# Kernel optimization log

Hardware: AMD Instinct MI355X
Metric: run time of the kernel (lower is better)

Reference implementation:

```python
import jax, jax.numpy as jnp
import numpy as np

B, S, E, H = 2, 2048, 1024, 16
DH = E // H


def setup_inputs() -> dict:
    key = jax.random.key(0)
    ks = jax.random.split(key, 12)
    std = 1.0 / np.sqrt(E)
    inp = {
        "query": jax.random.normal(ks[0], (B, S, E), jnp.float32),
        "key": jax.random.normal(ks[1], (B, S, E), jnp.float32),
        "value": jax.random.normal(ks[2], (B, S, E), jnp.float32),
        "mask": jax.random.randint(ks[3], (B, 1, 1, S), 0, 2, jnp.int32),
        "Wq": jax.random.normal(ks[4], (E, E), jnp.float32) * std,
        "bq": jnp.zeros((E,), jnp.float32),
        "Wk": jax.random.normal(ks[5], (E, E), jnp.float32) * std,
        "bk": jnp.zeros((E,), jnp.float32),
        "Wv": jax.random.normal(ks[6], (E, E), jnp.float32) * std,
        "bv": jnp.zeros((E,), jnp.float32),
        "Wo": jax.random.normal(ks[7], (E, E), jnp.float32) * std,
        "bo": jnp.zeros((E,), jnp.float32),
    }
    return inp


def reference(query, key, value, mask, Wq, bq, Wk, bk, Wv, bv, Wo, bo):
    b = query.shape[0]
    # QKV projections, then split heads: [B,S,E] -> [B,H,S,Dh]
    def split_heads(x):
        return x.reshape(b, -1, H, DH).transpose(0, 2, 1, 3)
    q = split_heads(query @ Wq + bq)
    k = split_heads(key @ Wk + bk)
    v = split_heads(value @ Wv + bv)
    # explicit bmm -> mask -> softmax -> bmm (non-SDPA), scores [B,H,Sq,Sk]
    scores = jnp.einsum("bhqd,bhkd->bhqk", q, k) / np.sqrt(DH).astype(np.float32)
    scores = jnp.where(mask == 0, jnp.float32(-1e9), scores)
    attn = jax.nn.softmax(scores, axis=-1)  # dropout is identity in eval mode
    out = jnp.einsum("bhqk,bhkd->bhqd", attn, v)
    out = out.transpose(0, 2, 1, 3).reshape(b, -1, E)  # merge heads
    return out @ Wo + bo
```

## Files before the change

kernel.cpp:

```cpp
#include <hip/hip_runtime.h>
#include <hip/hip_bf16.h>
#include <stdint.h>

#define B_ 2
#define S_ 2048
#define E_ 1024
#define H_ 16
#define DH_ 64
#define MELEMS (4096 * 1024)
#define WE (1024 * 1024)

typedef unsigned short u16;
typedef __bf16 bf16x8 __attribute__((ext_vector_type(8)));
typedef u16 u16x8 __attribute__((ext_vector_type(8)));
typedef u16 u16x4 __attribute__((ext_vector_type(4)));
typedef float f32x4 __attribute__((ext_vector_type(4)));
typedef float f32x16 __attribute__((ext_vector_type(16)));
typedef uint32_t u32x4 __attribute__((ext_vector_type(4)));
typedef uint32_t u32x2v __attribute__((ext_vector_type(2)));

__device__ __forceinline__ float bf2f(u16 u) {
    union { uint32_t i; float f; } v; v.i = ((uint32_t)u) << 16; return v.f;
}
__device__ __forceinline__ u16 f2bf(float f) {
    union { float f; uint32_t i; } v; v.f = f;
    uint32_t r = (v.i + 0x7FFFu + ((v.i >> 16) & 1u)) >> 16;
    return (u16)r;
}
__device__ __forceinline__ uint32_t cvtpk(float a, float b) {
    uint32_t r;
    asm("v_cvt_pk_bf16_f32 %0, %1, %2" : "=v"(r) : "v"(a), "v"(b));
    return r;
}
__device__ __forceinline__ bf16x8 ldfrag(const u16* p) {
    u16x8 t = *(const u16x8*)p;
    return __builtin_bit_cast(bf16x8, t);
}
__device__ __forceinline__ void gld16(const void* g, void* l) {
    __builtin_amdgcn_global_load_lds(
        (const __attribute__((address_space(1))) void*)g,
        (__attribute__((address_space(3))) void*)l, 16, 0, 0);
}

__global__ __launch_bounds__(256)
void cvt_all(const float* __restrict__ q, const float* __restrict__ k,
             const float* __restrict__ v,
             const float* __restrict__ W0, const float* __restrict__ W1,
             const float* __restrict__ W2, const float* __restrict__ W3,
             u16* __restrict__ Qi, u16* __restrict__ Ki, u16* __restrict__ Vi,
             u16* __restrict__ T0, u16* __restrict__ T1,
             u16* __restrict__ T2, u16* __restrict__ T3)
{
    __shared__ float tile[64][65];
    const int bid = blockIdx.x;
    const int tid = threadIdx.x;

    if (bid < 6144) {
        const int z = bid >> 11;
        const int cx = bid & 2047;
        const float* src = (z == 0) ? q : (z == 1) ? k : v;
        u16* dst = (z == 0) ? Qi : (z == 1) ? Ki : Vi;
        const size_t i8 = ((size_t)cx * 256 + tid) * 8;
        float4 f0 = *(const float4*)&src[i8];
        float4 f1 = *(const float4*)&src[i8 + 4];
        u16x8 t;
        t[0] = f2bf(f0.x); t[1] = f2bf(f0.y); t[2] = f2bf(f0.z); t[3] = f2bf(f0.w);
        t[4] = f2bf(f1.x); t[5] = f2bf(f1.y); t[6] = f2bf(f1.z); t[7] = f2bf(f1.w);
        *(u16x8*)&dst[i8] = t;
    } else {
        const int rr = bid - 6144;
        const int z = rr >> 8;
        const int tt = rr & 255;
        const float* W = (z == 0) ? W0 : (z == 1) ? W1 : (z == 2) ? W2 : W3;
        u16* T = (z == 0) ? T0 : (z == 1) ? T1 : (z == 2) ? T2 : T3;
        const int n0 = (tt & 15) * 64, k0 = (tt >> 4) * 64;
        const int r = tid >> 2, c0 = (tid & 3) * 16;

        #pragma unroll
        for (int i = 0; i < 4; ++i) {
            float4 w = *(const float4*)&W[(size_t)(k0 + r) * 1024 + n0 + c0 + i * 4];
            tile[r][c0 + i * 4 + 0] = w.x; tile[r][c0 + i * 4 + 1] = w.y;
            tile[r][c0 + i * 4 + 2] = w.z; tile[r][c0 + i * 4 + 3] = w.w;
        }
        __syncthreads();
        u16x8 a, b;
        #pragma unroll
        for (int j = 0; j < 8; ++j) a[j] = f2bf(tile[c0 + j][r]);
        #pragma unroll
        for (int j = 0; j < 8; ++j) b[j] = f2bf(tile[c0 + 8 + j][r]);
        *(u16x8*)&T[(size_t)(n0 + r) * 1024 + k0 + c0] = a;
        *(u16x8*)&T[(size_t)(n0 + r) * 1024 + k0 + c0 + 8] = b;
    }
}

template<int BN>
__global__ __launch_bounds__(256)
void gemm_bt(const u16* __restrict__ A0, const u16* __restrict__ A1,
             const u16* __restrict__ A2,
             const u16* __restrict__ Bt0, const u16* __restrict__ Bt1,
             const u16* __restrict__ Bt2,
             const float* __restrict__ b0, const float* __restrict__ b1,
             const float* __restrict__ b2,
             void* __restrict__ C0, void* __restrict__ C1, void* __restrict__ C2,
             const int* __restrict__ mask,
             int c_f32, int vt_z, float scale0, int K)
{
    const int z = blockIdx.z;
    const u16* A  = (z == 0) ? A0 : (z == 1) ? A1 : A2;
    const u16* Bt = (z == 0) ? Bt0 : (z == 1) ? Bt1 : Bt2;
    const float* bias = (z == 0) ? b0 : (z == 1) ? b1 : b2;
    void* C = (z == 0) ? C0 : (z == 1) ? C1 : C2;
    const float scale = (z == 0) ? scale0 : 1.0f;

    __shared__ alignas(16) u16 As[128 * 32];
    __shared__ alignas(16) u16 Bs[BN * 32];

    const int tid  = threadIdx.x;
    const int lane = tid & 63;
    const int wv   = tid >> 6;
    const int l15  = lane & 15;
    const int quad = lane >> 4;

    const int nwg = gridDim.x * gridDim.y;
    int wg = blockIdx.y * gridDim.x + blockIdx.x;
    wg = (wg & 7) * (nwg >> 3) + (wg >> 3);
    const int bx = wg % gridDim.x;
    const int by = wg / gridDim.x;

    const int m0 = by * 128;
    const int n0 = bx * BN;
    const int wr = (wv >> 1) * 64;
    const int wc = (wv & 1) * (BN / 2);

    const int srow = wv * 16 + (lane >> 2);
    const int skk  = (lane & 3) * 8;

    constexpr int NJ = BN / 32;
    f32x4 acc[4][NJ] = {};

    for (int k0 = 0; k0 < K; k0 += 32) {
        __syncthreads();
        #pragma unroll
        for (int h = 0; h < 2; ++h) {
            const int r = h * 64 + srow;
            gld16(&A[(size_t)(m0 + r) * K + k0 + skk], &As[r * 32 + skk]);
        }
        #pragma unroll
        for (int h = 0; h < BN / 64; ++h) {
            const int r = h * 64 + srow;
            gld16(&Bt[(size_t)(n0 + r) * K + k0 + skk], &Bs[r * 32 + skk]);
        }
        __syncthreads();

        bf16x8 a[4], b[NJ];
        #pragma unroll
        for (int i = 0; i < 4; ++i)
            a[i] = ldfrag(&As[(wr + i * 16 + l15) * 32 + quad * 8]);
        #pragma unroll
        for (int j = 0; j < NJ; ++j)
            b[j] = ldfrag(&Bs[(wc + j * 16 + l15) * 32 + quad * 8]);
        #pragma unroll
        for (int i = 0; i < 4; ++i)
            #pragma unroll
            for (int j = 0; j < NJ; ++j)
                acc[i][j] = __builtin_amdgcn_mfma_f32_16x16x32_bf16(
                    a[i], b[j], acc[i][j], 0, 0, 0);
    }

    #pragma unroll
    for (int j = 0; j < NJ; ++j) {
        const int col = n0 + wc + j * 16 + l15;
        const float bcol = bias[col];
        #pragma unroll
        for (int i = 0; i < 4; ++i) {
            const int row0 = m0 + wr + i * 16 + quad * 4;
            if (z == vt_z) {
                const int bb = row0 >> 11, s0 = row0 & 2047;
                const int4 mv = *(const int4*)&mask[bb * S_ + s0];
                u16x4 t;
                t[0] = mv.x ? f2bf((acc[i][j][0] + bcol) * scale) : (u16)0;
                t[1] = mv.y ? f2bf((acc[i][j][1] + bcol) * scale) : (u16)0;
                t[2] = mv.z ? f2bf((acc[i][j][2] + bcol) * scale) : (u16)0;
                t[3] = mv.w ? f2bf((acc[i][j][3] + bcol) * scale) : (u16)0;
                *(u16x4*)&((u16*)C)[((size_t)bb * E_ + col) * S_ + s0] = t;
            } else {
                #pragma unroll
                for (int r = 0; r < 4; ++r) {
                    const int row = row0 + r;
                    const float v = (acc[i][j][r] + bcol) * scale;
                    if (c_f32) ((float*)C)[(size_t)row * 1024 + col] = v;
                    else       ((u16*)C)[(size_t)row * 1024 + col]  = f2bf(v);
                }
            }
        }
    }
}

__global__ __launch_bounds__(512, 4)
void attn_v15(const u16* __restrict__ Q, const u16* __restrict__ K,
              const u16* __restrict__ Vt_g, const int* __restrict__ mask,
              u16* __restrict__ ctx)
{
    __shared__ alignas(16) u16 smem[2][8192];
    __shared__ alignas(16) u16 Mbf[S_];
    __shared__ float scrl[256];

    const int tid  = threadIdx.x;
    const int lane = tid & 63;
    const int wv   = tid >> 6;
    const int l31  = lane & 31;
    const int half = lane >> 5;
    const int sw7  = lane & 7;
    const int qw   = wv & 3;
    const int kh   = wv >> 2;
    const int kbase = kh * 32;

    const int nwg = gridDim.x * gridDim.y;
    int wg = blockIdx.y * gridDim.x + blockIdx.x;
    wg = (wg & 7) * (nwg >> 3) + (wg >> 3);
    const int qt = wg % gridDim.x;
    const int bh = wg / gridDim.x;
    const int b  = bh >> 4, h = bh & 15;

    const size_t qk_off = (size_t)b * S_ * E_ + (size_t)h * DH_;
    const size_t vt_off = ((size_t)b * E_ + (size_t)h * DH_) * S_;
    const int* mrow = &mask[b * S_];

    {
        const int i = tid * 4;
        const int4 m = *(const int4*)&mrow[i];
        u16x4 t;
        t[0] = m.x ? (u16)0x3F80 : (u16)0;
        t[1] = m.y ? (u16)0x3F80 : (u16)0;
        t[2] = m.z ? (u16)0x3F80 : (u16)0;
        t[3] = m.w ? (u16)0x3F80 : (u16)0;
        *(u16x4*)&Mbf[i] = t;
    }

    const int q0 = qt * 128 + qw * 32;
    bf16x8 qf[4];
    #pragma unroll
    for (int s = 0; s < 4; ++s)
        qf[s] = ldfrag(&Q[qk_off + (size_t)(q0 + l31) * E_ + s * 16 + half * 8]);

    f32x16 O[2] = {};
    f32x16 lacc = {};

    auto stage = [&](int kc, int buf) {
        const int rr = tid >> 3;
        const int ks = tid & 7;
        const int gb = ks ^ (rr & 7);
        gld16(&K[qk_off + (size_t)(kc + rr) * E_ + gb * 8],
              &smem[buf][rr * 64 + ks * 8]);
        gld16(&Vt_g[vt_off + (size_t)rr * S_ + kc + gb * 8],
              &smem[buf][4096 + rr * 64 + ks * 8]);
    };

    stage(0, 0);
    int cur = 0;

    for (int kc = 0; kc < S_; kc += 64) {
        __syncthreads();
        if (kc + 64 < S_) stage(kc + 64, cur ^ 1);
        const u16* Kb = &smem[cur][0];
        const u16* Vb = &smem[cur][4096];

        __builtin_amdgcn_s_setprio(1);
        f32x16 St = {};
        #pragma unroll
        for (int s = 0; s < 4; ++s) {
            bf16x8 kf = ldfrag(&Kb[(kbase + l31) * 64 + ((s * 2 + half) ^ sw7) * 8]);
            St = __builtin_amdgcn_mfma_f32_32x32x16_bf16(kf, qf[s], St, 0, 0, 0);
        }
        __builtin_amdgcn_s_setprio(0);
        float ex[16];
        #pragma unroll
        for (int i = 0; i < 16; ++i) ex[i] = __builtin_exp2f(St[i]);

        uint32_t wd[8];
        #pragma unroll
        for (int i = 0; i < 8; ++i) wd[i] = cvtpk(ex[2 * i], ex[2 * i + 1]);

        u32x2v r02 = __builtin_amdgcn_permlane32_swap(wd[0], wd[2], false, false);
        u32x2v r13 = __builtin_amdgcn_permlane32_swap(wd[1], wd[3], false, false);
        u32x2v r46 = __builtin_amdgcn_permlane32_swap(wd[4], wd[6], false, false);
        u32x2v r57 = __builtin_amdgcn_permlane32_swap(wd[5], wd[7], false, false);
        u32x4 f0, f1;
        f0[0] = r02[0]; f0[1] = r13[0]; f0[2] = r02[1]; f0[3] = r13[1];
        f1[0] = r46[0]; f1[1] = r57[0]; f1[2] = r46[1]; f1[3] = r57[1];
        const bf16x8 pa0 = __builtin_bit_cast(bf16x8, f0);
        const bf16x8 pa1 = __builtin_bit_cast(bf16x8, f1);

        __builtin_amdgcn_s_setprio(1);
        {
            bf16x8 mb0 = ldfrag(&Mbf[kc + kbase + half * 8]);
            bf16x8 mb1 = ldfrag(&Mbf[kc + kbase + 16 + half * 8]);
            lacc = __builtin_amdgcn_mfma_f32_32x32x16_bf16(pa0, mb0, lacc, 0, 0, 0);
            lacc = __builtin_amdgcn_mfma_f32_32x32x16_bf16(pa1, mb1, lacc, 0, 0, 0);
        }

        #pragma unroll
        for (int nt = 0; nt < 2; ++nt) {
            const int drow = nt * 32 + l31;
            const int kb0 = kh * 4 + half;
            const int kb1 = kh * 4 + 2 + half;
            bf16x8 vb0 = ldfrag(&Vb[drow * 64 + (kb0 ^ sw7) * 8]);
            bf16x8 vb1 = ldfrag(&Vb[drow * 64 + (kb1 ^ sw7) * 8]);
            O[nt] = __builtin_amdgcn_mfma_f32_32x32x16_bf16(pa0, vb0, O[nt], 0, 0, 0);
            O[nt] = __builtin_amdgcn_mfma_f32_32x32x16_bf16(pa1, vb1, O[nt], 0, 0, 0);
        }
        __builtin_amdgcn_s_setprio(0);
        cur ^= 1;
    }

    __syncthreads();
    float* scr = (float*)smem;
    const int sbase = (qw * 64 + lane) * 32;
    if (kh == 1) {
        #pragma unroll
        for (int j = 0; j < 4; ++j) {
            f32x4 t0, t1;
            #pragma unroll
            for (int r = 0; r < 4; ++r) { t0[r] = O[0][j * 4 + r]; t1[r] = O[1][j * 4 + r]; }
            *(f32x4*)&scr[sbase + (j ^ sw7) * 4]       = t0;
            *(f32x4*)&scr[sbase + ((j + 4) ^ sw7) * 4] = t1;
        }
        if (l31 == 0) {
            #pragma unroll
            for (int i = 0; i < 16; ++i)
                scrl[qw * 32 + half * 16 + i] = lacc[i];
        }
    }
    __syncthreads();
    if (kh == 0) {
        #pragma unroll
        for (int nt = 0; nt < 2; ++nt) {
            #pragma unroll
            for (int j = 0; j < 4; ++j) {
                const f32x4 p = *(const f32x4*)&scr[sbase + (((nt * 4 + j) ^ sw7)) * 4];
                #pragma unroll
                for (int r = 0; r < 4; ++r) {
                    const int i  = j * 4 + r;
                    const int ql = (i & 3) + 8 * (i >> 2) + 4 * half;
                    const float lt = lacc[i] + scrl[qw * 32 + half * 16 + i];
                    const float o  = O[nt][i] + p[r];
                    const int q = q0 + ql;
                    const int e = h * DH_ + nt * 32 + l31;
                    ctx[((size_t)b * S_ + q) * E_ + e] = f2bf(o / lt);
                }
            }
        }
    }
}

__global__ __launch_bounds__(256)
void gemm_bias(const void* __restrict__ A, int a_f32,
               const float* __restrict__ W, const float* __restrict__ bias,
               void* __restrict__ C, int c_f32,
               int M, int N, int K, float scale)
{
    __shared__ alignas(16) u16 As[64 * 32];
    __shared__ alignas(16) u16 Wt[64 * 32];
    const int tid  = threadIdx.x;
    const int lane = tid & 63;
    const int wv   = tid >> 6;
    const int l15  = lane & 15;
    const int quad = lane >> 4;
    const int m0 = blockIdx.y * 64, n0 = blockIdx.x * 64;
    const int wr = (wv >> 1) * 32, wc = (wv & 1) * 32;
    const int ar = tid >> 2, ac = (tid & 3) * 8;
    const int wk = tid >> 3, wn = (tid & 7) * 8;
    f32x4 acc[2][2] = {};
    for (int k0 = 0; k0 < K; k0 += 32) {
        __syncthreads();
        if (a_f32) {
            const float* Af = (const float*)A;
            const float* p = &Af[(size_t)(m0 + ar) * K + k0 + ac];
            float4 f0 = *(const float4*)p; float4 f1 = *(const float4*)(p + 4);
            u16x8 t;
            t[0] = f2bf(f0.x); t[1] = f2bf(f0.y); t[2] = f2bf(f0.z); t[3] = f2bf(f0.w);
            t[4] = f2bf(f1.x); t[5] = f2bf(f1.y); t[6] = f2bf(f1.z); t[7] = f2bf(f1.w);
            *(u16x8*)&As[ar * 32 + ac] = t;
        } else {
            const u16* Ab = (const u16*)A;
            *(u16x8*)&As[ar * 32 + ac] = *(const u16x8*)&Ab[(size_t)(m0 + ar) * K + k0 + ac];
        }
        {
            const float* p = &W[(size_t)(k0 + wk) * N + n0 + wn];
            float4 g0 = *(const float4*)p; float4 g1 = *(const float4*)(p + 4);
            float fv[8] = {g0.x, g0.y, g0.z, g0.w, g1.x, g1.y, g1.z, g1.w};
            #pragma unroll
            for (int j = 0; j < 8; ++j) Wt[(wn + j) * 32 + wk] = f2bf(fv[j]);
        }
        __syncthreads();
        bf16x8 a[2], b[2];
        #pragma unroll
        for (int sm = 0; sm < 2; ++sm) a[sm] = ldfrag(&As[(wr + sm * 16 + l15) * 32 + quad * 8]);
        #pragma unroll
        for (int sn = 0; sn < 2; ++sn) b[sn] = ldfrag(&Wt[(wc + sn * 16 + l15) * 32 + quad * 8]);
        #pragma unroll
        for (int sm = 0; sm < 2; ++sm)
            #pragma unroll
            for (int sn = 0; sn < 2; ++sn)
                acc[sm][sn] = __builtin_amdgcn_mfma_f32_16x16x32_bf16(a[sm], b[sn], acc[sm][sn], 0, 0, 0);
    }
    #pragma unroll
    for (int sm = 0; sm < 2; ++sm)
        #pragma unroll
        for (int sn = 0; sn < 2; ++sn) {
            const int col = n0 + wc + sn * 16 + l15;
            const float bcol = bias[col];
            #pragma unroll
            for (int r = 0; r < 4; ++r) {
                const int row = m0 + wr + sm * 16 + quad * 4 + r;
                const float v = (acc[sm][sn][r] + bcol) * scale;
                if (c_f32) ((float*)C)[(size_t)row * N + col] = v;
                else       ((u16*)C)[(size_t)row * N + col]  = f2bf(v);
            }
        }
}

__global__ __launch_bounds__(256)
void attn_v2(const u16* __restrict__ Q, const u16* __restrict__ K,
             const u16* __restrict__ V, const int* __restrict__ mask,
             u16* __restrict__ ctx, int BH_per_B)
{
    __shared__ alignas(16) u16 Ks[64 * 72];
    __shared__ alignas(16) u16 Vt[64 * 72];
    __shared__ alignas(16) u16 Pb[4][16 * 72];
    const int tid  = threadIdx.x;
    const int lane = tid & 63;
    const int wv   = tid >> 6;
    const int l15  = lane & 15;
    const int quad = lane >> 4;
    const int qt = blockIdx.x;
    const int bh = blockIdx.y;
    const int b  = bh / BH_per_B, h = bh % BH_per_B;
    const size_t headoff = (size_t)b * S_ * E_ + (size_t)h * DH_;
    const int qrow = qt * 64 + wv * 16 + l15;
    const bf16x8 qf0 = ldfrag(&Q[headoff + (size_t)qrow * E_ + quad * 8]);
    const bf16x8 qf1 = ldfrag(&Q[headoff + (size_t)qrow * E_ + 32 + quad * 8]);
    f32x4 oacc[4] = {};
    float mrun[4] = {-1e30f, -1e30f, -1e30f, -1e30f};
    float lrun[4] = {0.f, 0.f, 0.f, 0.f};
    const int skey = tid >> 2;
    const int sd0  = (tid & 3) * 16;
    for (int kc = 0; kc < S_; kc += 64) {
        __syncthreads();
        {
            const u16* kg = &K[headoff + (size_t)(kc + skey) * E_ + sd0];
            *(u16x8*)&Ks[skey * 72 + sd0]     = *(const u16x8*)kg;
            *(u16x8*)&Ks[skey * 72 + sd0 + 8] = *(const u16x8*)(kg + 8);
            const u16* vg = &V[headoff + (size_t)(kc + skey) * E_ + sd0];
            u16x8 v0 = *(const u16x8*)vg;
            u16x8 v1 = *(const u16x8*)(vg + 8);
            #pragma unroll
            for (int j = 0; j < 8; ++j) {
                const int d = sd0 + j;
                Vt[d * 72 + (skey ^ (((d >> 3) & 7) * 8))] = v0[j];
            }
            #pragma unroll
            for (int j = 0; j < 8; ++j) {
                const int d = sd0 + 8 + j;
                Vt[d * 72 + (skey ^ (((d >> 3) & 7) * 8))] = v1[j];
            }
        }
        __syncthreads();
        f32x4 sb[4];
        #pragma unroll
        for (int t = 0; t < 4; ++t) {
            bf16x8 kf0 = ldfrag(&Ks[(t * 16 + l15) * 72 + quad * 8]);
            bf16x8 kf1 = ldfrag(&Ks[(t * 16 + l15) * 72 + 32 + quad * 8]);
            f32x4 s = {};
            s = __builtin_amdgcn_mfma_f32_16x16x32_bf16(qf0, kf0, s, 0, 0, 0);
            s = __builtin_amdgcn_mfma_f32_16x16x32_bf16(qf1, kf1, s, 0, 0, 0);
            const int mv = mask[b * S_ + kc + t * 16 + l15];
            #pragma unroll
            for (int r = 0; r < 4; ++r) sb[t][r] = (mv == 0) ? -1e9f : s[r];
        }
        #pragma unroll
        for (int r = 0; r < 4; ++r) {
            float m = fmaxf(fmaxf(sb[0][r], sb[1][r]), fmaxf(sb[2][r], sb[3][r]));
            #pragma unroll
            for (int off = 1; off < 16; off <<= 1) m = fmaxf(m, __shfl_xor(m, off));
            const float mnew  = fmaxf(mrun[r], m);
            const float alpha = __expf(mrun[r] - mnew);
            mrun[r] = mnew;
            float sum = 0.f;
            #pragma unroll
            for (int t = 0; t < 4; ++t) {
                const float p = __expf(sb[t][r] - mnew);
                sb[t][r] = p; sum += p;
            }
            #pragma unroll
            for (int off = 1; off < 16; off <<= 1) sum += __shfl_xor(sum, off);
            lrun[r] = lrun[r] * alpha + sum;
            #pragma unroll
            for (int c = 0; c < 4; ++c) oacc[c][r] *= alpha;
        }
        #pragma unroll
        for (int t = 0; t < 4; ++t)
            #pragma unroll
            for (int r = 0; r < 4; ++r)
                Pb[wv][(quad * 4 + r) * 72 + t * 16 + l15] = f2bf(sb[t][r]);
        const bf16x8 pa0 = ldfrag(&Pb[wv][l15 * 72 + quad * 8]);
        const bf16x8 pa1 = ldfrag(&Pb[wv][l15 * 72 + 32 + quad * 8]);
        #pragma unroll
        for (int c = 0; c < 4; ++c) {
            const int d = c * 16 + l15;
            const int sg = ((d >> 3) & 7) * 8;
            bf16x8 vb0 = ldfrag(&Vt[d * 72 + ((quad * 8) ^ sg)]);
            bf16x8 vb1 = ldfrag(&Vt[d * 72 + ((32 + quad * 8) ^ sg)]);
            oacc[c] = __builtin_amdgcn_mfma_f32_16x16x32_bf16(pa0, vb0, oacc[c], 0, 0, 0);
            oacc[c] = __builtin_amdgcn_mfma_f32_16x16x32_bf16(pa1, vb1, oacc[c], 0, 0, 0);
        }
    }
    #pragma unroll
    for (int c = 0; c < 4; ++c) {
        const int e = h * DH_ + c * 16 + l15;
        #pragma unroll
        for (int r = 0; r < 4; ++r) {
            const int qg = qt * 64 + wv * 16 + quad * 4 + r;
            ctx[((size_t)b * S_ + qg) * E_ + e] = f2bf(oacc[c][r] / lrun[r]);
        }
    }
}

extern "C" void kernel_launch(void* const* d_in, const int* in_sizes, int n_in,
                              void* d_out, int out_size, void* d_ws, size_t ws_size,
                              hipStream_t stream)
{
    const float* query = (const float*)d_in[0];
    const float* key   = (const float*)d_in[1];
    const float* value = (const float*)d_in[2];
    const int*   mask  = (const int*)d_in[3];
    const float* Wq = (const float*)d_in[4];  const float* bq = (const float*)d_in[5];
    const float* Wk = (const float*)d_in[6];  const float* bk = (const float*)d_in[7];
    const float* Wv = (const float*)d_in[8];  const float* bv = (const float*)d_in[9];
    const float* Wo = (const float*)d_in[10]; const float* bo = (const float*)d_in[11];
    float* out = (float*)d_out;

    u16* ws = (u16*)d_ws;
    dim3 blk(256);

    const size_t need_fancy = (size_t)(6 * MELEMS + 4 * WE) * sizeof(u16);
    const size_t need_full  = (size_t)(4 * MELEMS) * sizeof(u16) + 64;

    if (ws_size >= need_fancy) {
        u16* Qi  = ws;
        u16* Ki  = Qi + MELEMS;
        u16* Vi  = Ki + MELEMS;
        u16* Wqt = Vi + MELEMS;
        u16* Wkt = Wqt + WE;
        u16* Wvt = Wkt + WE;
        u16* Wot = Wvt + WE;
        u16* Qp  = Wot + WE;
        u16* Kp  = Qp + MELEMS;
        u16* Vp  = Kp + MELEMS;
        u16* Cp  = Qi;

        cvt_all<<<dim3(7168), blk, 0, stream>>>(query, key, value,
                                                Wq, Wk, Wv, Wo,
                                                Qi, Ki, Vi, Wqt, Wkt, Wvt, Wot);

        gemm_bt<128><<<dim3(8, 32, 3), blk, 0, stream>>>(
            Qi, Ki, Vi, Wqt, Wkt, Wvt, bq, bk, bv,
            Qp, Kp, Vp, mask, 0, 2, 0.125f * 1.44269504f, E_);

        attn_v15<<<dim3(S_ / 128, B_ * H_), dim3(512), 0, stream>>>(
            Qp, Kp, Vp, mask, Cp);

        gemm_bt<64><<<dim3(16, 32, 1), blk, 0, stream>>>(
            Cp, Cp, Cp, Wot, Wot, Wot, bo, bo, bo,
            out, out, out, mask, 1, -1, 1.0f, E_);
    } else if (ws_size >= need_full) {
        u16* Qp = ws;
        u16* Kp = ws + MELEMS;
        u16* Vp = ws + 2 * MELEMS;
        u16* Cp = ws + 3 * MELEMS;
        const int M = B_ * S_;
        dim3 gg(E_ / 64, M / 64);
        gemm_bias<<<gg, blk, 0, stream>>>(query, 1, Wq, bq, Qp, 0, M, E_, E_, 0.125f);
        gemm_bias<<<gg, blk, 0, stream>>>(key,   1, Wk, bk, Kp, 0, M, E_, E_, 1.0f);
        gemm_bias<<<gg, blk, 0, stream>>>(value, 1, Wv, bv, Vp, 0, M, E_, E_, 1.0f);
        attn_v2<<<dim3(S_ / 64, B_ * H_), blk, 0, stream>>>(Qp, Kp, Vp, mask, Cp, H_);
        gemm_bias<<<gg, blk, 0, stream>>>(Cp, 0, Wo, bo, out, 1, M, E_, E_, 1.0f);
    } else {
        const size_t szb = (size_t)S_ * E_;
        u16* Qp = ws; u16* Kp = ws + szb; u16* Vp = ws + 2 * szb; u16* Cp = ws + 3 * szb;
        dim3 gg(E_ / 64, S_ / 64);
        for (int b = 0; b < B_; ++b) {
            gemm_bias<<<gg, blk, 0, stream>>>(query + b * szb, 1, Wq, bq, Qp, 0, S_, E_, E_, 0.125f);
            gemm_bias<<<gg, blk, 0, stream>>>(key   + b * szb, 1, Wk, bk, Kp, 0, S_, E_, E_, 1.0f);
            gemm_bias<<<gg, blk, 0, stream>>>(value + b * szb, 1, Wv, bv, Vp, 0, S_, E_, E_, 1.0f);
            attn_v2<<<dim3(S_ / 64, H_), blk, 0, stream>>>(Qp, Kp, Vp, mask + b * S_, Cp, H_);
            gemm_bias<<<gg, blk, 0, stream>>>(Cp, 0, Wo, bo, ((float*)d_out) + b * szb, 1, S_, E_, E_, 1.0f);
        }
    }
}
```

Measured before the change: 143.1 us.

## Fuse fp32-to-bf16 activation conversion into QKV projection GEMM A-loads

Removes the separate pass that converted query/key/value to bf16 in workspace. The QKV GEMM now reads fp32 activations directly into registers, converts them with packed bf16 conversion, and writes them to LDS. It also prefetches the next k-tile into registers while the MFMAs run. This drops one full read/write of the inputs and one kernel phase. In exchange the GEMM reads twice the A bytes per tile and uses more registers, and the async global-to-LDS load for A is lost.

```diff
diff --git a/kernel.cpp b/kernel.cpp
--- a/kernel.cpp
+++ b/kernel.cpp
@@ -43,60 +43,41 @@
 }
 
 __global__ __launch_bounds__(256)
-void cvt_all(const float* __restrict__ q, const float* __restrict__ k,
-             const float* __restrict__ v,
-             const float* __restrict__ W0, const float* __restrict__ W1,
-             const float* __restrict__ W2, const float* __restrict__ W3,
-             u16* __restrict__ Qi, u16* __restrict__ Ki, u16* __restrict__ Vi,
-             u16* __restrict__ T0, u16* __restrict__ T1,
-             u16* __restrict__ T2, u16* __restrict__ T3)
+void cvt_w(const float* __restrict__ W0, const float* __restrict__ W1,
+           const float* __restrict__ W2, const float* __restrict__ W3,
+           u16* __restrict__ T0, u16* __restrict__ T1,
+           u16* __restrict__ T2, u16* __restrict__ T3)
 {
     __shared__ float tile[64][65];
-    const int bid = blockIdx.x;
+    const int rr = blockIdx.x;
     const int tid = threadIdx.x;
-
-    if (bid < 6144) {
-        const int z = bid >> 11;
-        const int cx = bid & 2047;
-        const float* src = (z == 0) ? q : (z == 1) ? k : v;
-        u16* dst = (z == 0) ? Qi : (z == 1) ? Ki : Vi;
-        const size_t i8 = ((size_t)cx * 256 + tid) * 8;
-        float4 f0 = *(const float4*)&src[i8];
-        float4 f1 = *(const float4*)&src[i8 + 4];
-        u16x8 t;
-        t[0] = f2bf(f0.x); t[1] = f2bf(f0.y); t[2] = f2bf(f0.z); t[3] = f2bf(f0.w);
-        t[4] = f2bf(f1.x); t[5] = f2bf(f1.y); t[6] = f2bf(f1.z); t[7] = f2bf(f1.w);
-        *(u16x8*)&dst[i8] = t;
-    } else {
-        const int rr = bid - 6144;
-        const int z = rr >> 8;
-        const int tt = rr & 255;
-        const float* W = (z == 0) ? W0 : (z == 1) ? W1 : (z == 2) ? W2 : W3;
-        u16* T = (z == 0) ? T0 : (z == 1) ? T1 : (z == 2) ? T2 : T3;
-        const int n0 = (tt & 15) * 64, k0 = (tt >> 4) * 64;
-        const int r = tid >> 2, c0 = (tid & 3) * 16;
-
-        #pragma unroll
-        for (int i = 0; i < 4; ++i) {
-            float4 w = *(const float4*)&W[(size_t)(k0 + r) * 1024 + n0 + c0 + i * 4];
-            tile[r][c0 + i * 4 + 0] = w.x; tile[r][c0 + i * 4 + 1] = w.y;
-            tile[r][c0 + i * 4 + 2] = w.z; tile[r][c0 + i * 4 + 3] = w.w;
-        }
-        __syncthreads();
-        u16x8 a, b;
-        #pragma unroll
-        for (int j = 0; j < 8; ++j) a[j] = f2bf(tile[c0 + j][r]);
-        #pragma unroll
-        for (int j = 0; j < 8; ++j) b[j] = f2bf(tile[c0 + 8 + j][r]);
-        *(u16x8*)&T[(size_t)(n0 + r) * 1024 + k0 + c0] = a;
-        *(u16x8*)&T[(size_t)(n0 + r) * 1024 + k0 + c0 + 8] = b;
-    }
-}
-
-template<int BN>
+    const int z = rr >> 8;
+    const int tt = rr & 255;
+    const float* W = (z == 0) ? W0 : (z == 1) ? W1 : (z == 2) ? W2 : W3;
+    u16* T = (z == 0) ? T0 : (z == 1) ? T1 : (z == 2) ? T2 : T3;
+    const int n0 = (tt & 15) * 64, k0 = (tt >> 4) * 64;
+    const int r = tid >> 2, c0 = (tid & 3) * 16;
+
+    #pragma unroll
+    for (int i = 0; i < 4; ++i) {
+        float4 w = *(const float4*)&W[(size_t)(k0 + r) * 1024 + n0 + c0 + i * 4];
+        tile[r][c0 + i * 4 + 0] = w.x; tile[r][c0 + i * 4 + 1] = w.y;
+        tile[r][c0 + i * 4 + 2] = w.z; tile[r][c0 + i * 4 + 3] = w.w;
+    }
+    __syncthreads();
+    u16x8 a, b;
+    #pragma unroll
+    for (int j = 0; j < 8; ++j) a[j] = f2bf(tile[c0 + j][r]);
+    #pragma unroll
+    for (int j = 0; j < 8; ++j) b[j] = f2bf(tile[c0 + 8 + j][r]);
+    *(u16x8*)&T[(size_t)(n0 + r) * 1024 + k0 + c0] = a;
+    *(u16x8*)&T[(size_t)(n0 + r) * 1024 + k0 + c0 + 8] = b;
+}
+
+template<int BN, int AF32>
 __global__ __launch_bounds__(256)
-void gemm_bt(const u16* __restrict__ A0, const u16* __restrict__ A1,
-             const u16* __restrict__ A2,
+void gemm_bt(const void* __restrict__ A0, const void* __restrict__ A1,
+             const void* __restrict__ A2,
              const u16* __restrict__ Bt0, const u16* __restrict__ Bt1,
              const u16* __restrict__ Bt2,
              const float* __restrict__ b0, const float* __restrict__ b1,
@@ -106,7 +87,7 @@
              int c_f32, int vt_z, float scale0, int K)
 {
     const int z = blockIdx.z;
-    const u16* A  = (z == 0) ? A0 : (z == 1) ? A1 : A2;
+    const void* Av = (z == 0) ? A0 : (z == 1) ? A1 : A2;
     const u16* Bt = (z == 0) ? Bt0 : (z == 1) ? Bt1 : Bt2;
     const float* bias = (z == 0) ? b0 : (z == 1) ? b1 : b2;
     void* C = (z == 0) ? C0 : (z == 1) ? C1 : C2;
@@ -138,12 +119,33 @@
     constexpr int NJ = BN / 32;
     f32x4 acc[4][NJ] = {};
 
+    float4 ar0, ar1, ar2, ar3;
+    auto loadA = [&](int k0) {
+        const float* Af = (const float*)Av;
+        const float* p0 = &Af[(size_t)(m0 + srow) * K + k0 + skk];
+        const float* p1 = &Af[(size_t)(m0 + 64 + srow) * K + k0 + skk];
+        ar0 = *(const float4*)p0;  ar1 = *(const float4*)(p0 + 4);
+        ar2 = *(const float4*)p1;  ar3 = *(const float4*)(p1 + 4);
+    };
+    if (AF32) loadA(0);
+
     for (int k0 = 0; k0 < K; k0 += 32) {
         __syncthreads();
-        #pragma unroll
-        for (int h = 0; h < 2; ++h) {
-            const int r = h * 64 + srow;
-            gld16(&A[(size_t)(m0 + r) * K + k0 + skk], &As[r * 32 + skk]);
+        if (AF32) {
+            u32x4 w0, w1;
+            w0[0] = cvtpk(ar0.x, ar0.y); w0[1] = cvtpk(ar0.z, ar0.w);
+            w0[2] = cvtpk(ar1.x, ar1.y); w0[3] = cvtpk(ar1.z, ar1.w);
+            w1[0] = cvtpk(ar2.x, ar2.y); w1[1] = cvtpk(ar2.z, ar2.w);
+            w1[2] = cvtpk(ar3.x, ar3.y); w1[3] = cvtpk(ar3.z, ar3.w);
+            *(u32x4*)&As[srow * 32 + skk]        = w0;
+            *(u32x4*)&As[(64 + srow) * 32 + skk] = w1;
+        } else {
+            const u16* Ab = (const u16*)Av;
+            #pragma unroll
+            for (int h = 0; h < 2; ++h) {
+                const int r = h * 64 + srow;
+                gld16(&Ab[(size_t)(m0 + r) * K + k0 + skk], &As[r * 32 + skk]);
+            }
         }
         #pragma unroll
         for (int h = 0; h < BN / 64; ++h) {
@@ -159,6 +161,9 @@
         #pragma unroll
         for (int j = 0; j < NJ; ++j)
             b[j] = ldfrag(&Bs[(wc + j * 16 + l15) * 32 + quad * 8]);
+
+        if (AF32 && k0 + 32 < K) loadA(k0 + 32);
+
         #pragma unroll
         for (int i = 0; i < 4; ++i)
             #pragma unroll
@@ -548,9 +553,7 @@
 
     if (ws_size >= need_fancy) {
         u16* Qi  = ws;
-        u16* Ki  = Qi + MELEMS;
-        u16* Vi  = Ki + MELEMS;
-        u16* Wqt = Vi + MELEMS;
+        u16* Wqt = ws + 3 * (size_t)MELEMS;
         u16* Wkt = Wqt + WE;
         u16* Wvt = Wkt + WE;
         u16* Wot = Wvt + WE;
@@ -559,18 +562,17 @@
         u16* Vp  = Kp + MELEMS;
         u16* Cp  = Qi;
 
-        cvt_all<<<dim3(7168), blk, 0, stream>>>(query, key, value,
-                                                Wq, Wk, Wv, Wo,
-                                                Qi, Ki, Vi, Wqt, Wkt, Wvt, Wot);
-
-        gemm_bt<128><<<dim3(8, 32, 3), blk, 0, stream>>>(
-            Qi, Ki, Vi, Wqt, Wkt, Wvt, bq, bk, bv,
+        cvt_w<<<dim3(1024), blk, 0, stream>>>(Wq, Wk, Wv, Wo,
+                                              Wqt, Wkt, Wvt, Wot);
+
+        gemm_bt<128, 1><<<dim3(8, 32, 3), blk, 0, stream>>>(
+            query, key, value, Wqt, Wkt, Wvt, bq, bk, bv,
             Qp, Kp, Vp, mask, 0, 2, 0.125f * 1.44269504f, E_);
 
         attn_v15<<<dim3(S_ / 128, B_ * H_), dim3(512), 0, stream>>>(
             Qp, Kp, Vp, mask, Cp);
 
-        gemm_bt<64><<<dim3(16, 32, 1), blk, 0, stream>>>(
+        gemm_bt<64, 0><<<dim3(16, 32, 1), blk, 0, stream>>>(
             Cp, Cp, Cp, Wot, Wot, Wot, bo, bo, bo,
             out, out, out, mask, 1, -1, 1.0f, E_);
     } else if (ws_size >= need_full) {
```

New measurement: 134.5 us. -6.0%, faster.
